# Kernel optimization log

Hardware: AMD Instinct MI355X
Metric: run time of the kernel (lower is better)

Reference implementation:

```python
import jax, jax.numpy as jnp
import numpy as np

N_CHAN = 64
N_PTS = 2048
D_IN = 256
D_OUT = 256
N_FRAMES = 32  # config.n_frames; no_frames = N_FRAMES - 1


def setup_inputs() -> dict:
    key = jax.random.key(0)
    k1, k2, k3, k4, k5 = jax.random.split(key, 5)
    x = jax.random.normal(k1, (N_CHAN, N_PTS, D_IN), dtype=jnp.float32)
    t = jax.random.uniform(k2, (1, N_CHAN, 1), dtype=jnp.float32)
    model_idx = jax.random.randint(k3, (N_CHAN,), 0, N_CHAN)
    # per-channel weights, SIREN-style uniform init scale
    bound = 1.0 / np.sqrt(D_IN)
    W = jax.random.uniform(k4, (N_CHAN, D_IN, D_OUT), minval=-bound, maxval=bound, dtype=jnp.float32)
    B = jax.random.uniform(k5, (N_FRAMES, D_OUT), minval=-bound, maxval=bound, dtype=jnp.float32)
    return {"x": x, "t": t, "model_idx": model_idx, "W": W, "B": B}


def reference(x, t, model_idx, W, B):
    no_frames = N_FRAMES - 1
    # bias index per channel from the time coordinate: (t[0,:,0] * no_frames).long()
    bias_idx = (t[0, :, 0] * no_frames).astype(jnp.int32)  # [C]
    Wg = W[model_idx]          # [C, D_IN, D_OUT] gathered per-channel weights
    bg = B[bias_idx]           # [C, D_OUT] gathered per-channel biases
    # batched per-channel linear: x [C, N, D_IN] @ Wg [C, D_IN, D_OUT]
    out = jnp.einsum('cni,cio->cno', x, Wg) + bg[:, None, :]
    return out
```

## Files before the change

### kernel.cpp

```cpp
#include <hip/hip_runtime.h>


#define M_PTS 2048
#define K_DIM 256
#define N_DIM 256
#define BT_STRIDE 264
#define WT_BYTES ((size_t)64 * K_DIM * N_DIM * 2)

typedef float floatx4 __attribute__((ext_vector_type(4)));
typedef __bf16 bf16x4 __attribute__((ext_vector_type(4)));
typedef __bf16 bf16x8 __attribute__((ext_vector_type(8)));

typedef __attribute__((address_space(3))) void lds_void;
typedef const __attribute__((address_space(1))) void gbl_void;

__device__ __forceinline__ __bf16 cvt_bf16(float f) {
  unsigned u = __builtin_bit_cast(unsigned, f);
  unsigned r = (u + 0x7FFFu + ((u >> 16) & 1u)) >> 16;
  return __builtin_bit_cast(__bf16, (unsigned short)r);
}

__global__ __launch_bounds__(256) void wt_k(const float* __restrict__ W,
                                            const int* __restrict__ MI,
                                            __bf16* __restrict__ Wt) {
  __shared__ float tile[64][65];
  const int bid = blockIdx.x;
  const int c  = bid >> 4;
  const int kt = (bid >> 2) & 3;
  const int nt = bid & 3;
  const float* __restrict__ src =
      W + (size_t)MI[c] * (K_DIM * N_DIM) + (size_t)(kt * 64) * N_DIM + nt * 64;
  __bf16* __restrict__ dst =
      Wt + (size_t)c * (K_DIM * N_DIM) + (size_t)(nt * 64) * K_DIM + kt * 64;
  const int tid = threadIdx.x;
  {
    const int nl = tid & 63, kl0 = tid >> 6;
#pragma unroll
    for (int u = 0; u < 16; ++u)
      tile[kl0 + u * 4][nl] = src[(size_t)(kl0 + u * 4) * N_DIM + nl];
  }
  __syncthreads();
  {
    const int kl = tid & 63, nl0 = tid >> 6;
#pragma unroll
    for (int u = 0; u < 16; ++u)
      dst[(size_t)(nl0 + u * 4) * K_DIM + kl] = cvt_bf16(tile[kl][nl0 + u * 4]);
  }
}

__global__ __launch_bounds__(256, 4) void gemm_k(const float* __restrict__ X,
                                                 const float* __restrict__ T,
                                                 const __bf16* __restrict__ Wt,
                                                 const float* __restrict__ Bb,
                                                 float* __restrict__ Out) {
  __shared__ float As[2][128 * 32];

  const int bid = blockIdx.x;
  const int wg  = ((bid & 7) << 8) | (bid >> 3);
  const int c   = wg >> 5;
  const int mg  = (wg >> 1) & 15;
  const int nt  = wg & 1;
  const int n0  = nt * 128;
  const int m0  = mg * 128;

  const int tid  = threadIdx.x;
  const int lane = tid & 63;
  const int w    = tid >> 6;
  const int wm   = w & 1;
  const int wn   = w >> 1;
  const int r    = lane & 15;
  const int kg   = lane >> 4;

  const float*  __restrict__ Xc = X  + (size_t)c * (M_PTS * K_DIM);
  const __bf16* __restrict__ Wc = Wt + (size_t)c * (K_DIM * N_DIM);

  const int l8 = lane >> 3;
  const int lc = lane & 7;
  const float* __restrict__ xbase =
      Xc + (size_t)(m0 + w * 32 + l8) * K_DIM + ((lc ^ l8) << 2);
  const int lbase = (w * 32 + l8) * 32 + lc * 4;

#define STAGE(kt_, buf_)                                                      \
  {                                                                           \
    _Pragma("unroll") for (int u = 0; u < 4; ++u) {                           \
      __builtin_amdgcn_global_load_lds(                                       \
          (gbl_void*)(xbase + (size_t)u * 8 * K_DIM + (kt_) * 32),            \
          (lds_void*)(&As[buf_][lbase + u * 256]), 16, 0, 0);                 \
    }                                                                         \
  }

  const __bf16* __restrict__ wb[4];
#pragma unroll
  for (int j = 0; j < 4; ++j)
    wb[j] = Wc + (size_t)(n0 + wn * 64 + j * 16 + r) * K_DIM + kg * 8;

  int bidx = (int)(T[c] * 31.0f);
  bidx = bidx < 0 ? 0 : (bidx > 31 ? 31 : bidx);
  const float* __restrict__ brow = Bb + bidx * N_DIM + n0 + wn * 64;
  float bv[4];
#pragma unroll
  for (int j = 0; j < 4; ++j) bv[j] = brow[j * 16 + r];

  floatx4 acc[4][4] = {};

  STAGE(0, 0);
  int cur = 0;

  for (int kt = 0; kt < 8; ++kt) {
    __syncthreads();
    if (kt < 7) STAGE(kt + 1, cur ^ 1);

    bf16x8 b[4];
#pragma unroll
    for (int j = 0; j < 4; ++j) b[j] = *(const bf16x8*)(wb[j] + kt * 32);

    bf16x8 a[4];
#pragma unroll
    for (int i = 0; i < 4; ++i) {
      const int row = wm * 64 + i * 16 + r;
      const int p0  = ((kg * 32) ^ ((r & 7) << 4)) >> 2;
      const floatx4 f0 = *(const floatx4*)&As[cur][row * 32 + p0];
      const floatx4 f1 = *(const floatx4*)&As[cur][row * 32 + (p0 ^ 4)];
#pragma unroll
      for (int v = 0; v < 4; ++v) {
        a[i][v]     = cvt_bf16(f0[v]);
        a[i][v + 4] = cvt_bf16(f1[v]);
      }
    }

#pragma unroll
    for (int i = 0; i < 4; ++i)
#pragma unroll
      for (int j = 0; j < 4; ++j)
        acc[i][j] = __builtin_amdgcn_mfma_f32_16x16x32_bf16(a[i], b[j], acc[i][j], 0, 0, 0);

    cur ^= 1;
  }

  float* __restrict__ Oc = Out + (size_t)c * (M_PTS * N_DIM);
#pragma unroll
  for (int i = 0; i < 4; ++i) {
#pragma unroll
    for (int j = 0; j < 4; ++j) {
      const int col = n0 + wn * 64 + j * 16 + r;
#pragma unroll
      for (int v = 0; v < 4; ++v) {
        const int row = m0 + wm * 64 + i * 16 + kg * 4 + v;
        Oc[(size_t)row * N_DIM + col] = acc[i][j][v] + bv[j];
      }
    }
  }
#undef STAGE
}

__global__ __launch_bounds__(256) void fused_k(
    const float* __restrict__ X, const float* __restrict__ T,
    const int* __restrict__ MI, const float* __restrict__ W,
    const float* __restrict__ Bb, float* __restrict__ Out) {
  __shared__ __bf16 As[128 * 32];
  __shared__ __bf16 Bt[128 * BT_STRIDE];

  const int bid = blockIdx.x;
  const int c   = bid >> 4;
  const int mg  = (bid >> 1) & 7;
  const int nt  = bid & 1;
  const int n0  = nt * 128;

  const float* __restrict__ Xc = X + (size_t)c * (M_PTS * K_DIM);
  const float* __restrict__ Wc = W + (size_t)MI[c] * (K_DIM * N_DIM);

  const int tid  = threadIdx.x;
  const int lane = tid & 63;
  const int w    = tid >> 6;
  const int wm   = w & 1;
  const int wn   = w >> 1;
  const int r    = lane & 15;
  const int kg   = lane >> 4;

  {
    const int n  = tid & 127;
    const int kq = tid >> 7;
    const float* __restrict__ src = Wc + (size_t)(kq * 128) * N_DIM + n0 + n;
    __bf16* __restrict__ dst = &Bt[n * BT_STRIDE + kq * 128];
#pragma unroll 4
    for (int u = 0; u < 32; ++u) {
      bf16x4 v;
      v.x = cvt_bf16(src[(size_t)(u * 4 + 0) * N_DIM]);
      v.y = cvt_bf16(src[(size_t)(u * 4 + 1) * N_DIM]);
      v.z = cvt_bf16(src[(size_t)(u * 4 + 2) * N_DIM]);
      v.w = cvt_bf16(src[(size_t)(u * 4 + 3) * N_DIM]);
      *(bf16x4*)&dst[u * 4] = v;
    }
  }

  const int sm  = tid >> 1;
  const int skh = (tid & 1) * 16;
  const float* __restrict__ xrow = Xc + skh;
  __bf16* __restrict__ adst = &As[sm * 32 + skh];

  int bidx = (int)(T[c] * 31.0f);
  bidx = bidx < 0 ? 0 : (bidx > 31 ? 31 : bidx);
  const float* __restrict__ brow = Bb + bidx * N_DIM + n0 + wn * 64;
  float bv[4];
#pragma unroll
  for (int j = 0; j < 4; ++j) bv[j] = brow[j * 16 + r];

  float* __restrict__ Oc = Out + (size_t)c * (M_PTS * N_DIM);

  for (int mt2 = 0; mt2 < 2; ++mt2) {
    const int m0 = mg * 256 + mt2 * 128;
    const float* __restrict__ xsrc = xrow + (size_t)(m0 + sm) * K_DIM;
    floatx4 acc[4][4] = {};

    for (int kt = 0; kt < 8; ++kt) {
      const int k0 = kt * 32;
      __syncthreads();
      {
        floatx4 f0 = *(const floatx4*)(xsrc + k0 + 0);
        floatx4 f1 = *(const floatx4*)(xsrc + k0 + 4);
        floatx4 f2 = *(const floatx4*)(xsrc + k0 + 8);
        floatx4 f3 = *(const floatx4*)(xsrc + k0 + 12);
        bf16x8 h0, h1;
#pragma unroll
        for (int v = 0; v < 4; ++v) {
          h0[v]     = cvt_bf16(f0[v]);
          h0[v + 4] = cvt_bf16(f1[v]);
          h1[v]     = cvt_bf16(f2[v]);
          h1[v + 4] = cvt_bf16(f3[v]);
        }
        *(bf16x8*)&adst[0] = h0;
        *(bf16x8*)&adst[8] = h1;
      }
      __syncthreads();

      bf16x8 a[4], b[4];
#pragma unroll
      for (int i = 0; i < 4; ++i)
        a[i] = *(const bf16x8*)&As[(wm * 64 + i * 16 + r) * 32 + kg * 8];
#pragma unroll
      for (int j = 0; j < 4; ++j)
        b[j] = *(const bf16x8*)&Bt[(wn * 64 + j * 16 + r) * BT_STRIDE + k0 + kg * 8];
#pragma unroll
      for (int i = 0; i < 4; ++i)
#pragma unroll
        for (int j = 0; j < 4; ++j)
          acc[i][j] = __builtin_amdgcn_mfma_f32_16x16x32_bf16(a[i], b[j], acc[i][j], 0, 0, 0);
    }

#pragma unroll
    for (int i = 0; i < 4; ++i) {
#pragma unroll
      for (int j = 0; j < 4; ++j) {
        const int col = n0 + wn * 64 + j * 16 + r;
#pragma unroll
        for (int v = 0; v < 4; ++v) {
          const int row = m0 + wm * 64 + i * 16 + kg * 4 + v;
          Oc[(size_t)row * N_DIM + col] = acc[i][j][v] + bv[j];
        }
      }
    }
  }
}

extern "C" void kernel_launch(void* const* d_in, const int* in_sizes, int n_in,
                              void* d_out, int out_size, void* d_ws, size_t ws_size,
                              hipStream_t stream) {
  const float* X   = (const float*)d_in[0];
  const float* T   = (const float*)d_in[1];
  const int* MI    = (const int*)d_in[2];
  const float* W   = (const float*)d_in[3];
  const float* Bb  = (const float*)d_in[4];
  float* Out       = (float*)d_out;

  if (ws_size >= WT_BYTES && d_ws != nullptr) {
    __bf16* Wt = (__bf16*)d_ws;
    wt_k<<<dim3(1024), dim3(256), 0, stream>>>(W, MI, Wt);
    gemm_k<<<dim3(2048), dim3(256), 0, stream>>>(X, T, Wt, Bb, Out);
  } else {
    fused_k<<<dim3(1024), dim3(256), 0, stream>>>(X, T, MI, W, Bb, Out);
  }
}
```

Measured before the change: 274.3 us.

## Triple-buffer X tiles, prefetch W fragments, and use packed bf16 conversion in gemm_k

Switches the GEMM kernel from a double-buffered LDS pipeline to a triple-buffered one that stages two k-tiles ahead. The B fragments are register double-buffered through inline-asm global loads, and explicit vmcnt waits plus barriers control how far the loads run ahead. The software bf16 rounding is replaced by the hardware v_cvt_pk_bf16_f32 instruction. The aim is to hide global load latency and cut conversion ALU work. In exchange, occupancy is lowered to 3 blocks via launch bounds and more LDS is used, and correctness depends on the hand-counted waitcnt values.

```diff
diff --git a/kernel.cpp b/kernel.cpp
--- a/kernel.cpp
+++ b/kernel.cpp
@@ -8,6 +8,7 @@
 #define WT_BYTES ((size_t)64 * K_DIM * N_DIM * 2)
 
 typedef float floatx4 __attribute__((ext_vector_type(4)));
+typedef unsigned uintx4 __attribute__((ext_vector_type(4)));
 typedef __bf16 bf16x4 __attribute__((ext_vector_type(4)));
 typedef __bf16 bf16x8 __attribute__((ext_vector_type(8)));
 
@@ -18,6 +19,12 @@
   unsigned u = __builtin_bit_cast(unsigned, f);
   unsigned r = (u + 0x7FFFu + ((u >> 16) & 1u)) >> 16;
   return __builtin_bit_cast(__bf16, (unsigned short)r);
+}
+
+__device__ __forceinline__ unsigned cvt_pk(float lo, float hi) {
+  unsigned d;
+  asm("v_cvt_pk_bf16_f32 %0, %1, %2" : "=v"(d) : "v"(lo), "v"(hi));
+  return d;
 }
 
 __global__ __launch_bounds__(256) void wt_k(const float* __restrict__ W,
@@ -48,12 +55,12 @@
   }
 }
 
-__global__ __launch_bounds__(256, 4) void gemm_k(const float* __restrict__ X,
+__global__ __launch_bounds__(256, 3) void gemm_k(const float* __restrict__ X,
                                                  const float* __restrict__ T,
                                                  const __bf16* __restrict__ Wt,
                                                  const float* __restrict__ Bb,
                                                  float* __restrict__ Out) {
-  __shared__ float As[2][128 * 32];
+  __shared__ float As[3][128 * 32];
 
   const int bid = blockIdx.x;
   const int wg  = ((bid & 7) << 8) | (bid >> 3);
@@ -94,48 +101,72 @@
   for (int j = 0; j < 4; ++j)
     wb[j] = Wc + (size_t)(n0 + wn * 64 + j * 16 + r) * K_DIM + kg * 8;
 
+  floatx4 acc[4][4] = {};
+  uintx4 b0[4], b1[4];
+
+  STAGE(0, 0);
+  asm volatile("" ::: "memory");
+  STAGE(1, 1);
+  asm volatile("" ::: "memory");
+#pragma unroll
+  for (int j = 0; j < 4; ++j)
+    asm volatile("global_load_dwordx4 %0, %1, off"
+                 : "=&v"(b0[j]) : "v"(wb[j]) : "memory");
+
+#define STEP(s_, VTOP_, VMFMA_, BC_, BN_)                                     \
+  {                                                                           \
+    asm volatile("s_waitcnt vmcnt(" #VTOP_ ") lgkmcnt(0)" ::: "memory");      \
+    __builtin_amdgcn_sched_barrier(0);                                        \
+    __builtin_amdgcn_s_barrier();                                             \
+    __builtin_amdgcn_sched_barrier(0);                                        \
+    if ((s_) + 2 < 8) STAGE((s_) + 2, ((s_) + 2) % 3);                        \
+    asm volatile("" ::: "memory");                                            \
+    if ((s_) + 1 < 8) {                                                       \
+      _Pragma("unroll") for (int j = 0; j < 4; ++j)                           \
+        asm volatile("global_load_dwordx4 %0, %1, off"                        \
+                     : "=&v"(BN_[j])                                          \
+                     : "v"(wb[j] + ((s_) + 1) * 32) : "memory");              \
+    }                                                                         \
+    const float* __restrict__ Ab = As[(s_) % 3];                              \
+    floatx4 f0[4], f1[4];                                                     \
+    _Pragma("unroll") for (int i = 0; i < 4; ++i) {                           \
+      const int row_ = wm * 64 + i * 16 + r;                                  \
+      const int p0_  = ((kg * 32) ^ ((r & 7) << 4)) >> 2;                     \
+      f0[i] = *(const floatx4*)&Ab[row_ * 32 + p0_];                          \
+      f1[i] = *(const floatx4*)&Ab[row_ * 32 + (p0_ ^ 4)];                    \
+    }                                                                         \
+    asm volatile("s_waitcnt vmcnt(" #VMFMA_ ") lgkmcnt(0)" ::: "memory");     \
+    __builtin_amdgcn_sched_barrier(0);                                        \
+    _Pragma("unroll") for (int i = 0; i < 4; ++i) {                           \
+      uintx4 q;                                                               \
+      q.x = cvt_pk(f0[i].x, f0[i].y);                                         \
+      q.y = cvt_pk(f0[i].z, f0[i].w);                                         \
+      q.z = cvt_pk(f1[i].x, f1[i].y);                                         \
+      q.w = cvt_pk(f1[i].z, f1[i].w);                                         \
+      const bf16x8 av = __builtin_bit_cast(bf16x8, q);                        \
+      _Pragma("unroll") for (int j = 0; j < 4; ++j)                           \
+        acc[i][j] = __builtin_amdgcn_mfma_f32_16x16x32_bf16(                  \
+            av, __builtin_bit_cast(bf16x8, BC_[j]), acc[i][j], 0, 0, 0);      \
+    }                                                                         \
+  }
+
+  STEP(0,  8, 8, b0, b1);
+  STEP(1, 12, 8, b1, b0);
+  STEP(2, 12, 8, b0, b1);
+  STEP(3, 12, 8, b1, b0);
+  STEP(4, 12, 8, b0, b1);
+  STEP(5, 12, 8, b1, b0);
+  STEP(6, 12, 4, b0, b1);
+  STEP(7,  8, 0, b1, b0);
+#undef STEP
+#undef STAGE
+
   int bidx = (int)(T[c] * 31.0f);
   bidx = bidx < 0 ? 0 : (bidx > 31 ? 31 : bidx);
   const float* __restrict__ brow = Bb + bidx * N_DIM + n0 + wn * 64;
   float bv[4];
 #pragma unroll
   for (int j = 0; j < 4; ++j) bv[j] = brow[j * 16 + r];
-
-  floatx4 acc[4][4] = {};
-
-  STAGE(0, 0);
-  int cur = 0;
-
-  for (int kt = 0; kt < 8; ++kt) {
-    __syncthreads();
-    if (kt < 7) STAGE(kt + 1, cur ^ 1);
-
-    bf16x8 b[4];
-#pragma unroll
-    for (int j = 0; j < 4; ++j) b[j] = *(const bf16x8*)(wb[j] + kt * 32);
-
-    bf16x8 a[4];
-#pragma unroll
-    for (int i = 0; i < 4; ++i) {
-      const int row = wm * 64 + i * 16 + r;
-      const int p0  = ((kg * 32) ^ ((r & 7) << 4)) >> 2;
-      const floatx4 f0 = *(const floatx4*)&As[cur][row * 32 + p0];
-      const floatx4 f1 = *(const floatx4*)&As[cur][row * 32 + (p0 ^ 4)];
-#pragma unroll
-      for (int v = 0; v < 4; ++v) {
-        a[i][v]     = cvt_bf16(f0[v]);
-        a[i][v + 4] = cvt_bf16(f1[v]);
-      }
-    }
-
-#pragma unroll
-    for (int i = 0; i < 4; ++i)
-#pragma unroll
-      for (int j = 0; j < 4; ++j)
-        acc[i][j] = __builtin_amdgcn_mfma_f32_16x16x32_bf16(a[i], b[j], acc[i][j], 0, 0, 0);
-
-    cur ^= 1;
-  }
 
   float* __restrict__ Oc = Out + (size_t)c * (M_PTS * N_DIM);
 #pragma unroll
@@ -150,7 +181,6 @@
       }
     }
   }
-#undef STAGE
 }
 
 __global__ __launch_bounds__(256) void fused_k(
```

Measured after the change: 265.8 us. 3.1% less time.
